# Kernel tuning notes

Measured on AMD Instinct MI355X. Metric: run time of the kernel, lower is better.

## Reference

```python
import jax, jax.numpy as jnp
import numpy as np

B, C, H, W = 4, 256, 64, 64
PD = 32  # projection_dim = in_channels // projection_ratio


def setup_inputs() -> dict:
    key = jax.random.key(0)
    ks = jax.random.split(key, 7)
    x = jax.random.normal(ks[0], (B, C, H, W), dtype=jnp.float32)
    Wq = jax.random.normal(ks[1], (PD, C), dtype=jnp.float32) * (1.0 / np.sqrt(C))
    bq = jax.random.normal(ks[2], (PD,), dtype=jnp.float32) * 0.01
    Wk = jax.random.normal(ks[3], (PD, C), dtype=jnp.float32) * (1.0 / np.sqrt(C))
    bk = jax.random.normal(ks[4], (PD,), dtype=jnp.float32) * 0.01
    Wv = jax.random.normal(ks[5], (C, C), dtype=jnp.float32) * (1.0 / np.sqrt(C))
    bv = jax.random.normal(ks[6], (C,), dtype=jnp.float32) * 0.01
    gamma = jnp.float32(1.0)
    return {"x": x, "Wq": Wq, "bq": bq, "Wk": Wk, "bk": bk, "Wv": Wv, "bv": bv, "gamma": gamma}


def reference(x, Wq, bq, Wk, bk, Wv, bv, gamma):
    b, c, h, w = x.shape
    xf = x.reshape(b, c, h * w)                      # [B, C, N]
    q = jnp.einsum('dc,bcn->bnd', Wq, xf) + bq       # [B, N, PD]
    k = jnp.einsum('dc,bcn->bdn', Wk, xf) + bk[:, None]   # [B, PD, N]
    v = jnp.einsum('ec,bcn->ben', Wv, xf) + bv[:, None]   # [B, C, N]
    scores = jnp.einsum('bnd,bdm->bnm', q, k)        # [B, N, N] (no scaling, per original)
    attn = jax.nn.softmax(scores, axis=-1)           # softmax over keys
    out = jnp.einsum('bcn,bmn->bcm', v, attn)        # v @ attn^T -> [B, C, N]
    out = out.reshape(b, c, h, w)
    return gamma * out + x
```

## Files before the change

kernel.cpp:

```cpp
#include <hip/hip_runtime.h>
#include <stdint.h>

typedef _Float16 half_t;
typedef __attribute__((ext_vector_type(8))) _Float16 f16x8;
typedef __attribute__((ext_vector_type(4))) _Float16 f16x4;
typedef __attribute__((ext_vector_type(2))) __fp16 fp16x2;
typedef __attribute__((ext_vector_type(4))) float f32x4;
typedef __attribute__((ext_vector_type(16))) float f32x16;
typedef __attribute__((ext_vector_type(4))) uint32_t u32x4;
typedef __attribute__((ext_vector_type(2))) int i32x2;

#define DEVI __device__ __forceinline__

static constexpr int Bn = 4, Cc = 256, Nn = 4096, PD = 32;
static constexpr float L2E = 1.44269504089f;

__device__ half_t g_Q[(size_t)Bn * Nn * PD];
__device__ half_t g_K[(size_t)Bn * Nn * PD];
__device__ half_t g_V[(size_t)Bn * Cc * Nn];

DEVI f16x8 cvt8(float4 a, float4 b) {
    f16x8 r;
    r[0] = (_Float16)a.x; r[1] = (_Float16)a.y; r[2] = (_Float16)a.z; r[3] = (_Float16)a.w;
    r[4] = (_Float16)b.x; r[5] = (_Float16)b.y; r[6] = (_Float16)b.z; r[7] = (_Float16)b.w;
    return r;
}

DEVI uint32_t pkrtz(float a, float b) {
    fp16x2 h = __builtin_amdgcn_cvt_pkrtz(a, b);
    return __builtin_bit_cast(uint32_t, h);
}

DEVI float asf(int u) { return __builtin_bit_cast(float, u); }
DEVI int   asi(float f) { return __builtin_bit_cast(int, f); }

DEVI i32x2 pl32swap(int a, int b) {
    return __builtin_amdgcn_permlane32_swap(a, b, false, false);
}

DEVI void gll16(const void* g, void* l) {
    auto gp = (const __attribute__((address_space(1))) uint32_t*)(uintptr_t)g;
    auto lp = (__attribute__((address_space(3))) uint32_t*)(uintptr_t)l;
    __builtin_amdgcn_global_load_lds(gp, lp, 16, 0, 0);
}

__global__ __launch_bounds__(256, 1) void proj_kernel(
    const float* __restrict__ x,
    const float* __restrict__ Wq, const float* __restrict__ bq,
    const float* __restrict__ Wk, const float* __restrict__ bk,
    const float* __restrict__ Wv, const float* __restrict__ bv)
{
    __shared__ __align__(16) half_t xt[64 * 40];

    const int b    = blockIdx.x >> 6;
    const int n0   = (blockIdx.x & 63) * 64;
    const int t    = threadIdx.x;
    const int w    = t >> 6;
    const int lane = t & 63;
    const int l15  = lane & 15, g = lane >> 4;

    f32x4 qk_acc[4] = {};
    f32x4 v_acc[4][4] = {};

    const float* wrow_qk = (w < 2) ? (Wq + (size_t)(16 * w + l15) * Cc)
                                   : (Wk + (size_t)(16 * (w - 2) + l15) * Cc);

    for (int cs = 0; cs < 8; ++cs) {
        const int c0 = cs * 32;
        {
            const int nl = t & 63;
            const int cg = t >> 6;
            const float* xp = x + ((size_t)(b * Cc + c0 + cg * 8)) * Nn + n0 + nl;
            float f[8];
#pragma unroll
            for (int q = 0; q < 8; ++q) f[q] = xp[(size_t)q * Nn];
            f16x4 h0, h1;
#pragma unroll
            for (int q = 0; q < 4; ++q) { h0[q] = (_Float16)f[q]; h1[q] = (_Float16)f[q + 4]; }
            *(f16x4*)&xt[nl * 40 + cg * 8]     = h0;
            *(f16x4*)&xt[nl * 40 + cg * 8 + 4] = h1;
        }
        __syncthreads();

        f16x8 xf[4];
#pragma unroll
        for (int nf = 0; nf < 4; ++nf)
            xf[nf] = *(const f16x8*)&xt[(nf * 16 + l15) * 40 + g * 8];

        {
            const float* wp = wrow_qk + c0 + g * 8;
            const f16x8 af = cvt8(*(const float4*)wp, *(const float4*)(wp + 4));
#pragma unroll
            for (int nt = 0; nt < 4; ++nt)
                qk_acc[nt] = __builtin_amdgcn_mfma_f32_16x16x32_f16(af, xf[nt], qk_acc[nt], 0, 0, 0);
        }
#pragma unroll
        for (int et = 0; et < 4; ++et) {
            const int e = (w * 4 + et) * 16 + l15;
            const float* wp = Wv + (size_t)e * Cc + c0 + g * 8;
            const f16x8 wf = cvt8(*(const float4*)wp, *(const float4*)(wp + 4));
#pragma unroll
            for (int nf = 0; nf < 4; ++nf)
                v_acc[et][nf] = __builtin_amdgcn_mfma_f32_16x16x32_f16(xf[nf], wf, v_acc[et][nf], 0, 0, 0);
        }
        __syncthreads();
    }

    {
        const float* bias = (w < 2) ? bq : bk;
        const int dbase = 16 * (w & 1) + 4 * g;
        float bb[4];
#pragma unroll
        for (int r = 0; r < 4; ++r) bb[r] = bias[dbase + r];
        half_t* dst = (w < 2) ? g_Q : g_K;
#pragma unroll
        for (int nt = 0; nt < 4; ++nt) {
            const int n = n0 + nt * 16 + l15;
            f16x4 h;
#pragma unroll
            for (int r = 0; r < 4; ++r) h[r] = (_Float16)(qk_acc[nt][r] + bb[r]);
            *(f16x4*)&dst[((size_t)b * Nn + n) * PD + dbase] = h;
        }
    }
#pragma unroll
    for (int et = 0; et < 4; ++et) {
        const int e = (w * 4 + et) * 16 + l15;
        const float bve = bv[e];
#pragma unroll
        for (int nf = 0; nf < 4; ++nf) {
            const int n = n0 + nf * 16 + 4 * g;
            f16x4 h;
#pragma unroll
            for (int r = 0; r < 4; ++r) h[r] = (_Float16)(v_acc[et][nf][r] + bve);
            *(f16x4*)&g_V[((size_t)b * Cc + e) * Nn + n] = h;
        }
    }
}

__global__ __launch_bounds__(512, 2) void attn_kernel(
    const float* __restrict__ x, const float* __restrict__ gamma_p, float* __restrict__ out)
{
    __shared__ __align__(16) half_t V_lds[2][256 * 128];
    __shared__ float mx[2][4][32];
    __shared__ float lx[2][4][32];

    const int blk = blockIdx.x;
    const int grp = blk & 7;
    const int b   = grp >> 1;
    const int mt  = ((blk >> 3) << 1) | (grp & 1);

    const int t    = threadIdx.x;
    const int w    = t >> 6;
    const int lane = t & 63;
    const int l31  = lane & 31;
    const int hi   = lane >> 5;
    const int kk   = w & 3;
    const int mh   = w >> 2;
    const int mrow0 = mt * 64 + mh * 32;

    const half_t* Kb  = g_K + (size_t)b * Nn * PD;
    const half_t* Vbg = g_V + (size_t)b * Cc * Nn;

    const half_t* qp = g_Q + ((size_t)b * Nn + mrow0 + l31) * PD + hi * 8;
    const f16x8 q0 = *(const f16x8*)qp;
    const f16x8 q1 = *(const f16x8*)(qp + 16);

    const int vr = w * 4 + (lane >> 4);
    const half_t* vb = Vbg + (size_t)vr * Nn + (((lane & 15) ^ (vr & 7)) * 8);

    const int e7   = l31 & 7;
    const int off0 = (((kk * 4) + hi) ^ e7) * 8;
    const int off1 = (((kk * 4) + 2 + hi) ^ e7) * 8;

    f32x16 acc[8] = {};
    float run_m = -1e30f, run_l = 0.f;
    const f32x16 zero16 = {};

    f32x16 s;
    f16x8 kq0, kq1;

    {
        const half_t* kp0 = Kb + (size_t)(kk * 32 + l31) * PD + hi * 8;
        const f16x8 ka = *(const f16x8*)kp0;
        const f16x8 kb = *(const f16x8*)(kp0 + 16);
        s = __builtin_amdgcn_mfma_f32_32x32x16_f16(ka, q0, zero16, 0, 0, 0);
        s = __builtin_amdgcn_mfma_f32_32x32x16_f16(kb, q1, s, 0, 0, 0);
    }
#pragma unroll
    for (int rr = 0; rr < 8; ++rr)
        gll16(vb + (size_t)rr * 32 * Nn, &V_lds[0][rr * 4096 + w * 512]);
    vb += 128;
    const half_t* kp = Kb + (size_t)(128 + kk * 32 + l31) * PD + hi * 8;
    kq0 = *(const f16x8*)kp;
    kq1 = *(const f16x8*)(kp + 16);

    constexpr int NT = Nn / 128;
    for (int i = 0; i < NT; ++i) {
        const int buf = i & 1;
        const bool more = (i + 1 < NT);

        asm volatile("s_waitcnt vmcnt(2)" ::: "memory");
        __builtin_amdgcn_s_barrier();

        if (more) {
#pragma unroll
            for (int rr = 0; rr < 8; ++rr)
                gll16(vb + (size_t)rr * 32 * Nn, &V_lds[buf ^ 1][rr * 4096 + w * 512]);
            vb += 128;
        }

        f16x8 vfe[8];
#pragma unroll
        for (int et = 0; et < 4; ++et) {
            const int rowb = (et * 32 + l31) * 128;
            vfe[2 * et]     = *(const f16x8*)&V_lds[buf][rowb + off0];
            vfe[2 * et + 1] = *(const f16x8*)&V_lds[buf][rowb + off1];
        }

        float tm = s[0];
#pragma unroll
        for (int r = 1; r < 16; ++r) tm = fmaxf(tm, s[r]);
        {
            const i32x2 rr = pl32swap(asi(tm), asi(tm));
            tm = fmaxf(asf(rr[0]), asf(rr[1]));
        }
        float alpha = 1.f;
        if (__any(tm > run_m + 8.f)) {
            const float nm = fmaxf(run_m, tm);
            alpha = __builtin_amdgcn_exp2f((run_m - nm) * L2E);
            run_m = nm;
            float a16[16];
#pragma unroll
            for (int r = 0; r < 16; ++r)
                a16[r] = __shfl(alpha, (r & 3) + 8 * (r >> 2) + 4 * hi);
#pragma unroll
            for (int et = 0; et < 8; ++et)
#pragma unroll
                for (int r = 0; r < 16; ++r) acc[et][r] *= a16[r];
        }

        const float nms = run_m * L2E;
        float p[16];
#pragma unroll
        for (int r = 0; r < 16; ++r)
            p[r] = __builtin_amdgcn_exp2f(s[r] * L2E - nms);
        float rs = (((p[0] + p[1]) + (p[2] + p[3])) + ((p[4] + p[5]) + (p[6] + p[7])))
                 + (((p[8] + p[9]) + (p[10] + p[11])) + ((p[12] + p[13]) + (p[14] + p[15])));
        {
            const i32x2 rr = pl32swap(asi(rs), asi(rs));
            rs = asf(rr[0]) + asf(rr[1]);
        }
        run_l = run_l * alpha + rs;

        f16x8 pa0, pa1;
        {
            const i32x2 r0 = pl32swap((int)pkrtz(p[0], p[1]), (int)pkrtz(p[4], p[5]));
            const i32x2 r1 = pl32swap((int)pkrtz(p[2], p[3]), (int)pkrtz(p[6], p[7]));
            u32x4 d0 = {(uint32_t)r0[0], (uint32_t)r1[0], (uint32_t)r0[1], (uint32_t)r1[1]};
            pa0 = __builtin_bit_cast(f16x8, d0);
            const i32x2 r2 = pl32swap((int)pkrtz(p[8], p[9]),   (int)pkrtz(p[12], p[13]));
            const i32x2 r3 = pl32swap((int)pkrtz(p[10], p[11]), (int)pkrtz(p[14], p[15]));
            u32x4 d1 = {(uint32_t)r2[0], (uint32_t)r3[0], (uint32_t)r2[1], (uint32_t)r3[1]};
            pa1 = __builtin_bit_cast(f16x8, d1);
        }

        __builtin_amdgcn_s_setprio(1);
#pragma unroll
        for (int et = 0; et < 4; ++et) {
            acc[et] = __builtin_amdgcn_mfma_f32_32x32x16_f16(pa0, vfe[2 * et],     acc[et], 0, 0, 0);
            acc[et] = __builtin_amdgcn_mfma_f32_32x32x16_f16(pa1, vfe[2 * et + 1], acc[et], 0, 0, 0);
        }
        __builtin_amdgcn_s_setprio(0);

        __builtin_amdgcn_s_setprio(1);
#pragma unroll
        for (int et = 4; et < 8; ++et) {
            const int rowb = (et * 32 + l31) * 128;
            const f16x8 vf0 = *(const f16x8*)&V_lds[buf][rowb + off0];
            const f16x8 vf1 = *(const f16x8*)&V_lds[buf][rowb + off1];
            acc[et] = __builtin_amdgcn_mfma_f32_32x32x16_f16(pa0, vf0, acc[et], 0, 0, 0);
            acc[et] = __builtin_amdgcn_mfma_f32_32x32x16_f16(pa1, vf1, acc[et], 0, 0, 0);
        }
        __builtin_amdgcn_s_setprio(0);

        if (more) {
            s = __builtin_amdgcn_mfma_f32_32x32x16_f16(kq0, q0, zero16, 0, 0, 0);
            s = __builtin_amdgcn_mfma_f32_32x32x16_f16(kq1, q1, s, 0, 0, 0);
            kp += 128 * PD;
            if (i + 2 >= NT) kp = Kb + (size_t)(kk * 32 + l31) * PD + hi * 8;
            kq0 = *(const f16x8*)kp;
            kq1 = *(const f16x8*)(kp + 16);
        }
    }

    if (lane < 32) { mx[mh][kk][l31] = run_m; lx[mh][kk][l31] = run_l; }
    __syncthreads();

    float sc16[16], li16[16];
    {
        const float m0 = mx[mh][0][l31], m1 = mx[mh][1][l31];
        const float m2 = mx[mh][2][l31], m3 = mx[mh][3][l31];
        const float M  = fmaxf(fmaxf(m0, m1), fmaxf(m2, m3));
        const float L  = lx[mh][0][l31] * __builtin_amdgcn_exp2f((m0 - M) * L2E)
                       + lx[mh][1][l31] * __builtin_amdgcn_exp2f((m1 - M) * L2E)
                       + lx[mh][2][l31] * __builtin_amdgcn_exp2f((m2 - M) * L2E)
                       + lx[mh][3][l31] * __builtin_amdgcn_exp2f((m3 - M) * L2E);
        const float ssf = __builtin_amdgcn_exp2f((run_m - M) * L2E);
        const float inv = 1.0f / L;
#pragma unroll
        for (int r = 0; r < 16; ++r) {
            const int src = (r & 3) + 8 * (r >> 2) + 4 * hi;
            sc16[r] = __shfl(ssf, src);
            li16[r] = __shfl(inv, src);
        }
    }
    __syncthreads();

    const float gm = gamma_p[0];
    float4* mrg = (float4*)&V_lds[0][0];
#pragma unroll
    for (int h = 0; h < 2; ++h) {
#pragma unroll
        for (int j = 0; j < 4; ++j) {
            const int et = h * 4 + j;
#pragma unroll
            for (int q = 0; q < 4; ++q) {
                float4 v;
                v.x = acc[et][4 * q + 0] * sc16[4 * q + 0];
                v.y = acc[et][4 * q + 1] * sc16[4 * q + 1];
                v.z = acc[et][4 * q + 2] * sc16[4 * q + 2];
                v.w = acc[et][4 * q + 3] * sc16[4 * q + 3];
                mrg[((w * 4 + j) * 4 + q) * 64 + lane] = v;
            }
        }
        __syncthreads();
        {
            const int et = h * 4 + kk;
            const int e  = et * 32 + l31;
#pragma unroll
            for (int q = 0; q < 4; ++q) {
                float4 s0 = mrg[(((mh * 4 + 0) * 4 + kk) * 4 + q) * 64 + lane];
                float4 s1 = mrg[(((mh * 4 + 1) * 4 + kk) * 4 + q) * 64 + lane];
                float4 s2 = mrg[(((mh * 4 + 2) * 4 + kk) * 4 + q) * 64 + lane];
                float4 s3 = mrg[(((mh * 4 + 3) * 4 + kk) * 4 + q) * 64 + lane];
                const size_t idx = ((size_t)b * Cc + e) * Nn + mrow0 + 8 * q + 4 * hi;
                const float4 xin = *(const float4*)&x[idx];
                float4 o;
                o.x = gm * (s0.x + s1.x + s2.x + s3.x) * li16[4 * q + 0] + xin.x;
                o.y = gm * (s0.y + s1.y + s2.y + s3.y) * li16[4 * q + 1] + xin.y;
                o.z = gm * (s0.z + s1.z + s2.z + s3.z) * li16[4 * q + 2] + xin.z;
                o.w = gm * (s0.w + s1.w + s2.w + s3.w) * li16[4 * q + 3] + xin.w;
                *(float4*)&out[idx] = o;
            }
        }
        __syncthreads();
    }
}

extern "C" void kernel_launch(void* const* d_in, const int* in_sizes, int n_in,
                              void* d_out, int out_size, void* d_ws, size_t ws_size,
                              hipStream_t stream) {
    (void)in_sizes; (void)n_in; (void)out_size; (void)d_ws; (void)ws_size;
    const float* x  = (const float*)d_in[0];
    const float* Wq = (const float*)d_in[1];
    const float* bq = (const float*)d_in[2];
    const float* Wk = (const float*)d_in[3];
    const float* bk = (const float*)d_in[4];
    const float* Wv = (const float*)d_in[5];
    const float* bv = (const float*)d_in[6];
    const float* gm = (const float*)d_in[7];
    float* out = (float*)d_out;

    proj_kernel<<<256, 256, 0, stream>>>(x, Wq, bq, Wk, bk, Wv, bv);
    attn_kernel<<<256, 512, 0, stream>>>(x, gm, out);
}
```

Measured before the change: 83.19 us.

## Load V fragments directly from global memory instead of staging through LDS

```diff
diff --git a/kernel.cpp b/kernel.cpp
--- a/kernel.cpp
+++ b/kernel.cpp
@@ -38,12 +38,6 @@
     return __builtin_amdgcn_permlane32_swap(a, b, false, false);
 }
 
-DEVI void gll16(const void* g, void* l) {
-    auto gp = (const __attribute__((address_space(1))) uint32_t*)(uintptr_t)g;
-    auto lp = (__attribute__((address_space(3))) uint32_t*)(uintptr_t)l;
-    __builtin_amdgcn_global_load_lds(gp, lp, 16, 0, 0);
-}
-
 __global__ __launch_bounds__(256, 1) void proj_kernel(
     const float* __restrict__ x,
     const float* __restrict__ Wq, const float* __restrict__ bq,
@@ -140,7 +134,7 @@
 __global__ __launch_bounds__(512, 2) void attn_kernel(
     const float* __restrict__ x, const float* __restrict__ gamma_p, float* __restrict__ out)
 {
-    __shared__ __align__(16) half_t V_lds[2][256 * 128];
+    __shared__ __align__(16) float4 mrg_lds[32 * 4 * 64];
     __shared__ float mx[2][4][32];
     __shared__ float lx[2][4][32];
 
@@ -165,12 +159,7 @@
     const f16x8 q0 = *(const f16x8*)qp;
     const f16x8 q1 = *(const f16x8*)(qp + 16);
 
-    const int vr = w * 4 + (lane >> 4);
-    const half_t* vb = Vbg + (size_t)vr * Nn + (((lane & 15) ^ (vr & 7)) * 8);
-
-    const int e7   = l31 & 7;
-    const int off0 = (((kk * 4) + hi) ^ e7) * 8;
-    const int off1 = (((kk * 4) + 2 + hi) ^ e7) * 8;
+    const half_t* vp = Vbg + (size_t)l31 * Nn + kk * 32 + hi * 8;
 
     f32x16 acc[8] = {};
     float run_m = -1e30f, run_l = 0.f;
@@ -186,35 +175,21 @@
         s = __builtin_amdgcn_mfma_f32_32x32x16_f16(ka, q0, zero16, 0, 0, 0);
         s = __builtin_amdgcn_mfma_f32_32x32x16_f16(kb, q1, s, 0, 0, 0);
     }
-#pragma unroll
-    for (int rr = 0; rr < 8; ++rr)
-        gll16(vb + (size_t)rr * 32 * Nn, &V_lds[0][rr * 4096 + w * 512]);
-    vb += 128;
     const half_t* kp = Kb + (size_t)(128 + kk * 32 + l31) * PD + hi * 8;
     kq0 = *(const f16x8*)kp;
     kq1 = *(const f16x8*)(kp + 16);
 
     constexpr int NT = Nn / 128;
     for (int i = 0; i < NT; ++i) {
-        const int buf = i & 1;
         const bool more = (i + 1 < NT);
-
-        asm volatile("s_waitcnt vmcnt(2)" ::: "memory");
-        __builtin_amdgcn_s_barrier();
-
-        if (more) {
-#pragma unroll
-            for (int rr = 0; rr < 8; ++rr)
-                gll16(vb + (size_t)rr * 32 * Nn, &V_lds[buf ^ 1][rr * 4096 + w * 512]);
-            vb += 128;
-        }
+        const half_t* vtile = vp + (size_t)i * 128;
 
         f16x8 vfe[8];
 #pragma unroll
         for (int et = 0; et < 4; ++et) {
-            const int rowb = (et * 32 + l31) * 128;
-            vfe[2 * et]     = *(const f16x8*)&V_lds[buf][rowb + off0];
-            vfe[2 * et + 1] = *(const f16x8*)&V_lds[buf][rowb + off1];
+            const half_t* vq = vtile + (size_t)et * 32 * Nn;
+            vfe[2 * et]     = *(const f16x8*)vq;
+            vfe[2 * et + 1] = *(const f16x8*)(vq + 16);
         }
 
         float tm = s[0];
@@ -275,9 +250,9 @@
         __builtin_amdgcn_s_setprio(1);
 #pragma unroll
         for (int et = 4; et < 8; ++et) {
-            const int rowb = (et * 32 + l31) * 128;
-            const f16x8 vf0 = *(const f16x8*)&V_lds[buf][rowb + off0];
-            const f16x8 vf1 = *(const f16x8*)&V_lds[buf][rowb + off1];
+            const half_t* vq = vtile + (size_t)et * 32 * Nn;
+            const f16x8 vf0 = *(const f16x8*)vq;
+            const f16x8 vf1 = *(const f16x8*)(vq + 16);
             acc[et] = __builtin_amdgcn_mfma_f32_32x32x16_f16(pa0, vf0, acc[et], 0, 0, 0);
             acc[et] = __builtin_amdgcn_mfma_f32_32x32x16_f16(pa1, vf1, acc[et], 0, 0, 0);
         }
@@ -286,10 +261,11 @@
         if (more) {
             s = __builtin_amdgcn_mfma_f32_32x32x16_f16(kq0, q0, zero16, 0, 0, 0);
             s = __builtin_amdgcn_mfma_f32_32x32x16_f16(kq1, q1, s, 0, 0, 0);
-            kp += 128 * PD;
-            if (i + 2 >= NT) kp = Kb + (size_t)(kk * 32 + l31) * PD + hi * 8;
-            kq0 = *(const f16x8*)kp;
-            kq1 = *(const f16x8*)(kp + 16);
+            if (i + 2 < NT) {
+                kp += 128 * PD;
+                kq0 = *(const f16x8*)kp;
+                kq1 = *(const f16x8*)(kp + 16);
+            }
         }
     }
 
@@ -314,10 +290,9 @@
             li16[r] = __shfl(inv, src);
         }
     }
-    __syncthreads();
 
     const float gm = gamma_p[0];
-    float4* mrg = (float4*)&V_lds[0][0];
+    float4* mrg = mrg_lds;
 #pragma unroll
     for (int h = 0; h < 2; ++h) {
 #pragma unroll
```

Result: slower. 167.7 us (+101.6%).
